# Performance work log

Hardware: AMD Instinct MI355X
Metric: run time of the kernel (lower is better)

## Reference

```python
import jax, jax.numpy as jnp
import numpy as np

NUM_SEGMENTS = 1024  # number of graphs in the batch (max batch id + 1)
D = 256              # input_dim
H = D // 2           # attention hidden dim
N = 500000           # total nodes


def setup_inputs() -> dict:
    key = jax.random.key(0)
    k1, k2, k3, k4, k5 = jax.random.split(key, 5)
    x = jax.random.normal(k1, (N, D), dtype=jnp.float32)
    batch = jnp.sort(jax.random.randint(k2, (N,), 0, NUM_SEGMENTS))
    # attention_net params (Linear(D, D//2), Tanh, Linear(D//2, 1))
    s1 = 1.0 / np.sqrt(D)
    s2 = 1.0 / np.sqrt(H)
    W1 = jax.random.uniform(k3, (D, H), jnp.float32, -s1, s1)
    b1 = jnp.zeros((H,), jnp.float32)
    W2 = jax.random.uniform(k4, (H, 1), jnp.float32, -s2, s2)
    b2 = jnp.zeros((1,), jnp.float32)
    return {"x": x, "batch": batch, "W1": W1, "b1": b1, "W2": W2, "b2": b2}


def reference(x, batch, W1, b1, W2, b2):
    # MLP attention scores: [N, 1]
    scores = jnp.tanh(x @ W1 + b1) @ W2 + b2
    s = scores[:, 0]  # [N]
    # per-segment softmax (numerically stable)
    seg_max = jax.ops.segment_max(s, batch, num_segments=NUM_SEGMENTS)  # [G]
    e = jnp.exp(s - seg_max[batch])
    denom = jax.ops.segment_sum(e, batch, num_segments=NUM_SEGMENTS)   # [G]
    w = e / denom[batch]  # [N], sums to 1 per segment
    # global_mean_pool(x * w, batch): segment sum / segment count
    weighted = x * w[:, None]  # [N, D]
    seg_sum = jax.ops.segment_sum(weighted, batch, num_segments=NUM_SEGMENTS)  # [G, D]
    counts = jax.ops.segment_sum(jnp.ones_like(s), batch, num_segments=NUM_SEGMENTS)
    return seg_sum / jnp.maximum(counts, 1.0)[:, None]
```

## Files before the change

### kernel.cpp

```cpp
#include <hip/hip_runtime.h>
#include <hip/hip_bf16.h>

constexpr int DD   = 256;
constexpr int HH   = 128;
constexpr int NSEG = 1024;

typedef __attribute__((ext_vector_type(8))) short short8;
typedef __attribute__((ext_vector_type(4))) float f32x4;

__device__ __forceinline__ short f2bf(float f) {
  unsigned u = __float_as_uint(f);
  u = (u + 0x7FFFu + ((u >> 16) & 1u)) >> 16;
  return (short)u;
}
__device__ __forceinline__ unsigned fenc(float f) {
  unsigned u = __float_as_uint(f);
  return (u & 0x80000000u) ? ~u : (u | 0x80000000u);
}
__device__ __forceinline__ float fdec(unsigned u) {
  return (u & 0x80000000u) ? __uint_as_float(u & 0x7FFFFFFFu) : __uint_as_float(~u);
}

__global__ __launch_bounds__(256) void k0_init(unsigned* __restrict__ segmaxu,
                                               float* __restrict__ denom,
                                               float* __restrict__ accbuf) {
  int i = blockIdx.x * 256 + threadIdx.x;
  if (i < NSEG) { segmaxu[i] = 0u; denom[i] = 0.f; }
  if (i < NSEG * DD) accbuf[i] = 0.f;
}

__global__ __launch_bounds__(256) void k1_scores(
    const float* __restrict__ x, const int* __restrict__ batch,
    const float* __restrict__ W1, const float* __restrict__ b1,
    const float* __restrict__ W2, const float* __restrict__ b2,
    float* __restrict__ scores, unsigned* __restrict__ segmaxu, int N) {
  constexpr int KP = DD + 8;
  __shared__ __align__(16) short w1t[HH * KP];
  __shared__ float sb1[HH], sw2[HH];

  for (int idx = threadIdx.x; idx < DD * HH; idx += 256) {
    int k = idx >> 7, h = idx & 127;
    w1t[h * KP + k] = f2bf(W1[idx]);
  }
  if (threadIdx.x < HH) {
    sb1[threadIdx.x] = b1[threadIdx.x];
    sw2[threadIdx.x] = W2[threadIdx.x];
  }
  __syncthreads();

  const float b2v = b2[0];
  const int l = threadIdx.x & 63;
  const int w = threadIdx.x >> 6;
  const int c = l & 15;
  const int q = l >> 4;

  for (int rt = 0; rt < 8; rt++) {
    int rowt = blockIdx.x * 512 + w * 128 + rt * 16;
    if (rowt >= N) break;

    int arow = rowt + c;
    if (arow > N - 1) arow = N - 1;
    const float* xrow = x + (size_t)arow * DD + q * 8;

    short8 af[8];
#pragma unroll
    for (int kk = 0; kk < 8; kk++) {
      float4 a0 = *(const float4*)(xrow + kk * 32);
      float4 a1 = *(const float4*)(xrow + kk * 32 + 4);
      short8 pk;
      pk[0] = f2bf(a0.x); pk[1] = f2bf(a0.y); pk[2] = f2bf(a0.z); pk[3] = f2bf(a0.w);
      pk[4] = f2bf(a1.x); pk[5] = f2bf(a1.y); pk[6] = f2bf(a1.z); pk[7] = f2bf(a1.w);
      af[kk] = pk;
    }

    f32x4 acc[8] = {};
#pragma unroll
    for (int kk = 0; kk < 8; kk++) {
#pragma unroll
      for (int t = 0; t < 8; t++) {
        short8 bf = *(const short8*)&w1t[(t * 16 + c) * KP + kk * 32 + q * 8];
        acc[t] = __builtin_amdgcn_mfma_f32_16x16x32_bf16(af[kk], bf, acc[t], 0, 0, 0);
      }
    }

    float part[4] = {0.f, 0.f, 0.f, 0.f};
#pragma unroll
    for (int t = 0; t < 8; t++) {
      float w2c = sw2[t * 16 + c];
      float b1c = sb1[t * 16 + c];
#pragma unroll
      for (int r = 0; r < 4; r++) {
        float v = acc[t][r] + b1c;
        float e2 = __expf(2.f * v);
        part[r] += (1.f - 2.f / (e2 + 1.f)) * w2c;
      }
    }
#pragma unroll
    for (int r = 0; r < 4; r++) {
      part[r] += __shfl_xor(part[r], 1, 64);
      part[r] += __shfl_xor(part[r], 2, 64);
      part[r] += __shfl_xor(part[r], 4, 64);
      part[r] += __shfl_xor(part[r], 8, 64);
    }
    if (c == 0) {
#pragma unroll
      for (int r = 0; r < 4; r++) {
        int row = rowt + q * 4 + r;
        if (row < N) {
          float s = part[r] + b2v;
          scores[row] = s;
          atomicMax(&segmaxu[batch[row]], fenc(s));
        }
      }
    }
  }
}

__global__ __launch_bounds__(256) void k3_wsum(
    const float* __restrict__ x, const int* __restrict__ batch,
    const float* __restrict__ scores, const unsigned* __restrict__ segmaxu,
    float* __restrict__ accbuf, float* __restrict__ denom, int N) {
  const int l = threadIdx.x & 63;
  const int w = threadIdx.x >> 6;
  const int base = blockIdx.x * 256;
  const float4* x4 = (const float4*)x;

  float4 facc = make_float4(0.f, 0.f, 0.f, 0.f);
  float dsum = 0.f;
  int prevseg = -1;
  float m = 0.f;

  for (int i = 0; i < 64; i++) {
    int row = base + w + i * 4;
    if (row >= N) break;
    int seg = batch[row];
    if (seg != prevseg) {
      if (prevseg >= 0) {
        float* ap = accbuf + prevseg * DD + l * 4;
        atomicAdd(ap + 0, facc.x); atomicAdd(ap + 1, facc.y);
        atomicAdd(ap + 2, facc.z); atomicAdd(ap + 3, facc.w);
        if (l == 0) atomicAdd(&denom[prevseg], dsum);
      }
      facc = make_float4(0.f, 0.f, 0.f, 0.f);
      dsum = 0.f;
      prevseg = seg;
      m = fdec(segmaxu[seg]);
    }
    float e = __expf(scores[row] - m);
    float4 xv = x4[(size_t)row * 64 + l];
    facc.x += e * xv.x; facc.y += e * xv.y;
    facc.z += e * xv.z; facc.w += e * xv.w;
    dsum += e;
  }
  if (prevseg >= 0) {
    float* ap = accbuf + prevseg * DD + l * 4;
    atomicAdd(ap + 0, facc.x); atomicAdd(ap + 1, facc.y);
    atomicAdd(ap + 2, facc.z); atomicAdd(ap + 3, facc.w);
    if (l == 0) atomicAdd(&denom[prevseg], dsum);
  }
}

__global__ __launch_bounds__(256) void k4_final(
    const int* __restrict__ batch, const float* __restrict__ accbuf,
    const float* __restrict__ denom, float* __restrict__ out, int N) {
  int seg = blockIdx.x;
  int lo = 0, hi = N;
  while (lo < hi) { int mid = (lo + hi) >> 1; if (batch[mid] < seg) lo = mid + 1; else hi = mid; }
  int lb = lo;
  hi = N;
  while (lo < hi) { int mid = (lo + hi) >> 1; if (batch[mid] <= seg) lo = mid + 1; else hi = mid; }
  int cnt = lo - lb;
  float v = 0.f;
  if (cnt > 0) v = accbuf[seg * DD + threadIdx.x] / (denom[seg] * (float)cnt);
  out[seg * DD + threadIdx.x] = v;
}

extern "C" void kernel_launch(void* const* d_in, const int* in_sizes, int n_in,
                              void* d_out, int out_size, void* d_ws, size_t ws_size,
                              hipStream_t stream) {
  const float* x     = (const float*)d_in[0];
  const int*   batch = (const int*)d_in[1];
  const float* W1    = (const float*)d_in[2];
  const float* b1    = (const float*)d_in[3];
  const float* W2    = (const float*)d_in[4];
  const float* b2    = (const float*)d_in[5];
  float* out = (float*)d_out;
  const int N = in_sizes[1];

  float*    ws      = (float*)d_ws;
  float*    scores  = ws;
  unsigned* segmaxu = (unsigned*)(ws + N);
  float*    denom   = ws + N + NSEG;
  float*    accbuf  = ws + N + 2 * NSEG;

  hipLaunchKernelGGL(k0_init, dim3((NSEG * DD + 255) / 256), dim3(256), 0, stream,
                     segmaxu, denom, accbuf);
  hipLaunchKernelGGL(k1_scores, dim3((N + 511) / 512), dim3(256), 0, stream,
                     x, batch, W1, b1, W2, b2, scores, segmaxu, N);
  hipLaunchKernelGGL(k3_wsum, dim3((N + 255) / 256), dim3(256), 0, stream,
                     x, batch, scores, segmaxu, accbuf, denom, N);
  hipLaunchKernelGGL(k4_final, dim3(NSEG), dim3(256), 0, stream,
                     batch, accbuf, denom, out, N);
}
```

Before: 946.7 us.

## Fuse score and weighted-sum passes with per-block online softmax partials

Merges the score MLP kernel and the weighted segment-sum kernel into one block-local pass. Each block computes per-run local maxima, exp sums and x accumulators and writes them to per-block partial slots, and a final kernel merges the partials with a rescaled log-sum-exp. This avoids a second read of x from HBM, the global atomic max and the accumulator init kernel. W1 is pre-converted once to a swizzled bf16 layout that blocks copy straight into LDS, and activations are converted with packed bf16 convert instructions. Blocks whose 512 rows span more than MAXR segments would clamp run ids and merge different segments into one slot, and the partial buffers use more workspace.

```diff
diff --git a/kernel.cpp b/kernel.cpp
--- a/kernel.cpp
+++ b/kernel.cpp
@@ -4,14 +4,16 @@
 constexpr int DD   = 256;
 constexpr int HH   = 128;
 constexpr int NSEG = 1024;
+constexpr int BR   = 512;
+constexpr int MAXR = 8;
 
 typedef __attribute__((ext_vector_type(8))) short short8;
 typedef __attribute__((ext_vector_type(4))) float f32x4;
 
-__device__ __forceinline__ short f2bf(float f) {
+__device__ __forceinline__ unsigned short f2bf(float f) {
   unsigned u = __float_as_uint(f);
   u = (u + 0x7FFFu + ((u >> 16) & 1u)) >> 16;
-  return (short)u;
+  return (unsigned short)u;
 }
 __device__ __forceinline__ unsigned fenc(float f) {
   unsigned u = __float_as_uint(f);
@@ -21,45 +23,51 @@
   return (u & 0x80000000u) ? __uint_as_float(u & 0x7FFFFFFFu) : __uint_as_float(~u);
 }
 
-__global__ __launch_bounds__(256) void k0_init(unsigned* __restrict__ segmaxu,
-                                               float* __restrict__ denom,
-                                               float* __restrict__ accbuf) {
-  int i = blockIdx.x * 256 + threadIdx.x;
-  if (i < NSEG) { segmaxu[i] = 0u; denom[i] = 0.f; }
-  if (i < NSEG * DD) accbuf[i] = 0.f;
-}
-
-__global__ __launch_bounds__(256) void k1_scores(
+__global__ __launch_bounds__(256) void kprep(const float* __restrict__ W1,
+                                             unsigned short* __restrict__ w1p) {
+  int id = blockIdx.x * 256 + threadIdx.x;
+  int h = id >> 8, k = id & 255;
+  int sidx = (h * 256 + k) ^ ((h & 7) << 3);
+  w1p[sidx] = f2bf(W1[k * HH + h]);
+}
+
+__global__ __launch_bounds__(512, 4) void ka(
     const float* __restrict__ x, const int* __restrict__ batch,
-    const float* __restrict__ W1, const float* __restrict__ b1,
+    const unsigned short* __restrict__ w1p, const float* __restrict__ b1,
     const float* __restrict__ W2, const float* __restrict__ b2,
-    float* __restrict__ scores, unsigned* __restrict__ segmaxu, int N) {
-  constexpr int KP = DD + 8;
-  __shared__ __align__(16) short w1t[HH * KP];
+    int* __restrict__ pseg, float* __restrict__ pm, float* __restrict__ psum,
+    float* __restrict__ pacc, int N) {
+  __shared__ __align__(16) unsigned short w1t[HH * DD];
+  __shared__ float se_lds[BR];
+  __shared__ int   batch_lds[BR];
+  __shared__ short rid_lds[BR];
   __shared__ float sb1[HH], sw2[HH];
-
-  for (int idx = threadIdx.x; idx < DD * HH; idx += 256) {
-    int k = idx >> 7, h = idx & 127;
-    w1t[h * KP + k] = f2bf(W1[idx]);
-  }
-  if (threadIdx.x < HH) {
-    sb1[threadIdx.x] = b1[threadIdx.x];
-    sw2[threadIdx.x] = W2[threadIdx.x];
-  }
+  __shared__ unsigned runmax_u[MAXR];
+  __shared__ float runsum[MAXR];
+  __shared__ int wtot[8], woff[8];
+
+  const int t = threadIdx.x, b = blockIdx.x;
+  const int l = t & 63, w = t >> 6;
+  const int c = l & 15, q = l >> 4;
+
+  {
+    const float4* src = (const float4*)w1p;
+    float4* dst = (float4*)w1t;
+#pragma unroll
+    for (int rnd = 0; rnd < 8; rnd++) dst[rnd * 512 + t] = src[rnd * 512 + t];
+  }
+  if (t < HH) { sb1[t] = b1[t]; sw2[t] = W2[t]; }
+  {
+    int row = b * BR + t;
+    batch_lds[t] = batch[row < N ? row : (N - 1)];
+  }
+  if (t < MAXR) { runmax_u[t] = 0u; runsum[t] = 0.f; }
   __syncthreads();
 
   const float b2v = b2[0];
-  const int l = threadIdx.x & 63;
-  const int w = threadIdx.x >> 6;
-  const int c = l & 15;
-  const int q = l >> 4;
-
-  for (int rt = 0; rt < 8; rt++) {
-    int rowt = blockIdx.x * 512 + w * 128 + rt * 16;
-    if (rowt >= N) break;
-
-    int arow = rowt + c;
-    if (arow > N - 1) arow = N - 1;
+  for (int rt = 0; rt < 4; rt++) {
+    int rowt = b * BR + w * 64 + rt * 16;
+    int arow = rowt + c; if (arow > N - 1) arow = N - 1;
     const float* xrow = x + (size_t)arow * DD + q * 8;
 
     short8 af[8];
@@ -67,30 +75,32 @@
     for (int kk = 0; kk < 8; kk++) {
       float4 a0 = *(const float4*)(xrow + kk * 32);
       float4 a1 = *(const float4*)(xrow + kk * 32 + 4);
-      short8 pk;
-      pk[0] = f2bf(a0.x); pk[1] = f2bf(a0.y); pk[2] = f2bf(a0.z); pk[3] = f2bf(a0.w);
-      pk[4] = f2bf(a1.x); pk[5] = f2bf(a1.y); pk[6] = f2bf(a1.z); pk[7] = f2bf(a1.w);
-      af[kk] = pk;
+      union { short8 v; unsigned u[4]; } pk;
+      asm("v_cvt_pk_bf16_f32 %0, %1, %2" : "=v"(pk.u[0]) : "v"(a0.x), "v"(a0.y));
+      asm("v_cvt_pk_bf16_f32 %0, %1, %2" : "=v"(pk.u[1]) : "v"(a0.z), "v"(a0.w));
+      asm("v_cvt_pk_bf16_f32 %0, %1, %2" : "=v"(pk.u[2]) : "v"(a1.x), "v"(a1.y));
+      asm("v_cvt_pk_bf16_f32 %0, %1, %2" : "=v"(pk.u[3]) : "v"(a1.z), "v"(a1.w));
+      af[kk] = pk.v;
     }
 
     f32x4 acc[8] = {};
 #pragma unroll
     for (int kk = 0; kk < 8; kk++) {
 #pragma unroll
-      for (int t = 0; t < 8; t++) {
-        short8 bf = *(const short8*)&w1t[(t * 16 + c) * KP + kk * 32 + q * 8];
-        acc[t] = __builtin_amdgcn_mfma_f32_16x16x32_bf16(af[kk], bf, acc[t], 0, 0, 0);
+      for (int tt = 0; tt < 8; tt++) {
+        int idx = ((tt * 16 + c) * 256 + kk * 32 + q * 8) ^ ((c & 7) << 3);
+        short8 bf = *(const short8*)&w1t[idx];
+        acc[tt] = __builtin_amdgcn_mfma_f32_16x16x32_bf16(af[kk], bf, acc[tt], 0, 0, 0);
       }
     }
 
     float part[4] = {0.f, 0.f, 0.f, 0.f};
 #pragma unroll
-    for (int t = 0; t < 8; t++) {
-      float w2c = sw2[t * 16 + c];
-      float b1c = sb1[t * 16 + c];
+    for (int tt = 0; tt < 8; tt++) {
+      float w2c = sw2[tt * 16 + c], b1c = sb1[tt * 16 + c];
 #pragma unroll
       for (int r = 0; r < 4; r++) {
-        float v = acc[t][r] + b1c;
+        float v = acc[tt][r] + b1c;
         float e2 = __expf(2.f * v);
         part[r] += (1.f - 2.f / (e2 + 1.f)) * w2c;
       }
@@ -105,74 +115,114 @@
     if (c == 0) {
 #pragma unroll
       for (int r = 0; r < 4; r++) {
-        int row = rowt + q * 4 + r;
-        if (row < N) {
-          float s = part[r] + b2v;
-          scores[row] = s;
-          atomicMax(&segmaxu[batch[row]], fenc(s));
-        }
-      }
-    }
-  }
-}
-
-__global__ __launch_bounds__(256) void k3_wsum(
-    const float* __restrict__ x, const int* __restrict__ batch,
-    const float* __restrict__ scores, const unsigned* __restrict__ segmaxu,
-    float* __restrict__ accbuf, float* __restrict__ denom, int N) {
-  const int l = threadIdx.x & 63;
-  const int w = threadIdx.x >> 6;
-  const int base = blockIdx.x * 256;
+        int rl = w * 64 + rt * 16 + q * 4 + r;
+        int row = b * BR + rl;
+        se_lds[rl] = (row < N) ? (part[r] + b2v) : -1e30f;
+      }
+    }
+  }
+  __syncthreads();
+
+  int seg = batch_lds[t];
+  bool flag = (t == 0) || (seg != batch_lds[t - 1]);
+  unsigned long long bal = __ballot(flag ? 1 : 0);
+  int pre = __popcll(bal & ((1ull << l) - 1ull));
+  if (l == 63) wtot[w] = pre + (flag ? 1 : 0);
+  __syncthreads();
+  if (t == 0) {
+    int sacc = 0;
+    for (int i = 0; i < 8; i++) { woff[i] = sacc; sacc += wtot[i]; }
+  }
+  __syncthreads();
+  int rid = woff[w] + pre + (flag ? 1 : 0) - 1;
+  if (rid > MAXR - 1) rid = MAXR - 1;
+  rid_lds[t] = (short)rid;
+
+  float* myacc = pacc + (size_t)b * (MAXR * DD);
+  for (int i = t; i < MAXR * DD; i += BR) myacc[i] = 0.f;
+
+  float s = se_lds[t];
+  atomicMax(&runmax_u[rid], fenc(s));
+  __syncthreads();
+  float m = fdec(runmax_u[rid]);
+  int myrow = b * BR + t;
+  float e = (myrow < N) ? __expf(s - m) : 0.f;
+  se_lds[t] = e;
+  atomicAdd(&runsum[rid], e);
+  __syncthreads();
+  if (flag) {
+    int slot = b * MAXR + rid;
+    pseg[slot] = seg;
+    pm[slot]   = m;
+    psum[slot] = runsum[rid];
+  }
+
   const float4* x4 = (const float4*)x;
-
   float4 facc = make_float4(0.f, 0.f, 0.f, 0.f);
-  float dsum = 0.f;
-  int prevseg = -1;
-  float m = 0.f;
-
+  int prid = rid_lds[w * 64];
   for (int i = 0; i < 64; i++) {
-    int row = base + w + i * 4;
-    if (row >= N) break;
-    int seg = batch[row];
-    if (seg != prevseg) {
-      if (prevseg >= 0) {
-        float* ap = accbuf + prevseg * DD + l * 4;
-        atomicAdd(ap + 0, facc.x); atomicAdd(ap + 1, facc.y);
-        atomicAdd(ap + 2, facc.z); atomicAdd(ap + 3, facc.w);
-        if (l == 0) atomicAdd(&denom[prevseg], dsum);
-      }
+    int tl = w * 64 + i;
+    int rid2 = rid_lds[tl];
+    if (rid2 != prid) {
+      float* ap = myacc + prid * DD + l * 4;
+      atomicAdd(ap + 0, facc.x); atomicAdd(ap + 1, facc.y);
+      atomicAdd(ap + 2, facc.z); atomicAdd(ap + 3, facc.w);
       facc = make_float4(0.f, 0.f, 0.f, 0.f);
-      dsum = 0.f;
-      prevseg = seg;
-      m = fdec(segmaxu[seg]);
-    }
-    float e = __expf(scores[row] - m);
-    float4 xv = x4[(size_t)row * 64 + l];
-    facc.x += e * xv.x; facc.y += e * xv.y;
-    facc.z += e * xv.z; facc.w += e * xv.w;
-    dsum += e;
-  }
-  if (prevseg >= 0) {
-    float* ap = accbuf + prevseg * DD + l * 4;
+      prid = rid2;
+    }
+    int row = b * BR + tl;
+    if (row < N) {
+      float ev = se_lds[tl];
+      float4 xv = x4[(size_t)row * 64 + l];
+      facc.x += ev * xv.x; facc.y += ev * xv.y;
+      facc.z += ev * xv.z; facc.w += ev * xv.w;
+    }
+  }
+  {
+    float* ap = myacc + prid * DD + l * 4;
     atomicAdd(ap + 0, facc.x); atomicAdd(ap + 1, facc.y);
     atomicAdd(ap + 2, facc.z); atomicAdd(ap + 3, facc.w);
-    if (l == 0) atomicAdd(&denom[prevseg], dsum);
-  }
-}
-
-__global__ __launch_bounds__(256) void k4_final(
-    const int* __restrict__ batch, const float* __restrict__ accbuf,
-    const float* __restrict__ denom, float* __restrict__ out, int N) {
-  int seg = blockIdx.x;
-  int lo = 0, hi = N;
-  while (lo < hi) { int mid = (lo + hi) >> 1; if (batch[mid] < seg) lo = mid + 1; else hi = mid; }
-  int lb = lo;
-  hi = N;
-  while (lo < hi) { int mid = (lo + hi) >> 1; if (batch[mid] <= seg) lo = mid + 1; else hi = mid; }
-  int cnt = lo - lb;
-  float v = 0.f;
-  if (cnt > 0) v = accbuf[seg * DD + threadIdx.x] / (denom[seg] * (float)cnt);
-  out[seg * DD + threadIdx.x] = v;
+  }
+}
+
+__global__ __launch_bounds__(256) void kb(
+    const int* __restrict__ batch, const int* __restrict__ pseg,
+    const float* __restrict__ pm, const float* __restrict__ psum,
+    const float* __restrict__ pacc, float* __restrict__ out, int N) {
+  int s = blockIdx.x, d = threadIdx.x;
+  __shared__ int slb, sub;
+  if (d == 0) {
+    int lo = 0, hi = N;
+    while (lo < hi) { int mid = (lo + hi) >> 1; if (batch[mid] < s) lo = mid + 1; else hi = mid; }
+    slb = lo;
+    hi = N;
+    while (lo < hi) { int mid = (lo + hi) >> 1; if (batch[mid] <= s) lo = mid + 1; else hi = mid; }
+    sub = lo;
+  }
+  __syncthreads();
+  int lb = slb, ub = sub, cnt = ub - lb;
+  float res = 0.f;
+  if (cnt > 0) {
+    int b0 = lb / BR, b1 = (ub - 1) / BR;
+    float mg = -3e38f;
+    for (int b = b0; b <= b1; b++)
+      for (int r = 0; r < MAXR; r++) {
+        int sl = b * MAXR + r;
+        if (pseg[sl] == s) mg = fmaxf(mg, pm[sl]);
+      }
+    float den = 0.f, num = 0.f;
+    for (int b = b0; b <= b1; b++)
+      for (int r = 0; r < MAXR; r++) {
+        int sl = b * MAXR + r;
+        if (pseg[sl] == s) {
+          float sc = __expf(pm[sl] - mg);
+          den += sc * psum[sl];
+          num += sc * pacc[(size_t)sl * DD + d];
+        }
+      }
+    res = num / (den * (float)cnt);
+  }
+  out[s * DD + d] = res;
 }
 
 extern "C" void kernel_launch(void* const* d_in, const int* in_sizes, int n_in,
@@ -186,19 +236,18 @@
   const float* b2    = (const float*)d_in[5];
   float* out = (float*)d_out;
   const int N = in_sizes[1];
-
-  float*    ws      = (float*)d_ws;
-  float*    scores  = ws;
-  unsigned* segmaxu = (unsigned*)(ws + N);
-  float*    denom   = ws + N + NSEG;
-  float*    accbuf  = ws + N + 2 * NSEG;
-
-  hipLaunchKernelGGL(k0_init, dim3((NSEG * DD + 255) / 256), dim3(256), 0, stream,
-                     segmaxu, denom, accbuf);
-  hipLaunchKernelGGL(k1_scores, dim3((N + 511) / 512), dim3(256), 0, stream,
-                     x, batch, W1, b1, W2, b2, scores, segmaxu, N);
-  hipLaunchKernelGGL(k3_wsum, dim3((N + 255) / 256), dim3(256), 0, stream,
-                     x, batch, scores, segmaxu, accbuf, denom, N);
-  hipLaunchKernelGGL(k4_final, dim3(NSEG), dim3(256), 0, stream,
-                     batch, accbuf, denom, out, N);
-}
+  const int nblk = (N + BR - 1) / BR;
+
+  char* wsb = (char*)d_ws;
+  unsigned short* w1p  = (unsigned short*)wsb;
+  float*          pacc = (float*)(wsb + 65536);
+  float*          pm   = pacc + (size_t)nblk * MAXR * DD;
+  float*          psum = pm + (size_t)nblk * MAXR;
+  int*            pseg = (int*)(psum + (size_t)nblk * MAXR);
+
+  hipLaunchKernelGGL(kprep, dim3(HH * DD / 256), dim3(256), 0, stream, W1, w1p);
+  hipLaunchKernelGGL(ka, dim3(nblk), dim3(512), 0, stream,
+                     x, batch, w1p, b1, W2, b2, pseg, pm, psum, pacc, N);
+  hipLaunchKernelGGL(kb, dim3(NSEG), dim3(256), 0, stream,
+                     batch, pseg, pm, psum, pacc, out, N);
+}
```

Result: faster. 799.8 us (-15.5%).
